# Performance work log

Measured on AMD Instinct MI355X. Metric: run time of the kernel, lower is better.

Reference implementation:

```python
import jax, jax.numpy as jnp
import numpy as np

B, H, W, C = 8, 224, 224, 64
KH = KW = 3          # patch size
RANK = 100           # low rank
FILTERS = 256
IN_DIM = KH * KW * C  # 576


def extract_patches_same(x):
    """tf.image.extract_patches, sizes=3x3, strides=1, rates=1, SAME.

    Output channel ordering matches TF: [kh, kw, C] (spatial-major).
    x: (B,H,W,C) -> (B,H,W,KH*KW*C)
    """
    xp = jnp.pad(x, ((0, 0), (1, 1), (1, 1), (0, 0)))
    slices = [xp[:, di:di + H, dj:dj + W, :]
              for di in range(KH) for dj in range(KW)]
    return jnp.concatenate(slices, axis=-1)


def setup_inputs() -> dict:
    key = jax.random.key(0)
    ks = jax.random.split(key, 11)
    std = 0.05  # keras 'random_normal' initializer stddev
    return {
        "x": jax.random.normal(ks[0], (B, H, W, C), jnp.float32),
        "k": jax.random.normal(ks[1], (IN_DIM, RANK), jnp.float32) * std,
        "l_t": jax.random.normal(ks[2], (RANK, FILTERS), jnp.float32) * std,
        "s": jax.random.normal(ks[3], (RANK, RANK), jnp.float32) * std,
        "aux_U": jax.random.normal(ks[4], (IN_DIM, RANK), jnp.float32) * std,
        "aux_Unp1": jax.random.normal(ks[5], (IN_DIM, RANK), jnp.float32) * std,
        "aux_Vt": jax.random.normal(ks[6], (RANK, FILTERS), jnp.float32) * std,
        "aux_Vtnp1": jax.random.normal(ks[7], (RANK, FILTERS), jnp.float32) * std,
        "b": jax.random.normal(ks[8], (H, W, FILTERS), jnp.float32) * std,
        "aux_b": jax.random.normal(ks[9], (H, W, FILTERS), jnp.float32) * std,
        "step": 2,
    }


def reference(x, k, l_t, s, aux_U, aux_Unp1, aux_Vt, aux_Vtnp1, b, aux_b, step):
    patches = extract_patches_same(x)  # (B,H,W,IN_DIM)
    if step == 0:
        z = jnp.einsum('bhwp,pr->bhwr', patches, k)
        z = jnp.einsum('bhwr,rf->bhwf', z, aux_Vt) + aux_b
    elif step == 1:
        z = jnp.einsum('bhwp,pr->bhwr', patches, aux_U)
        z = jnp.einsum('bhwr,rf->bhwf', z, l_t) + aux_b
    else:
        z = jnp.einsum('bhwp,pr->bhwr', patches, aux_Unp1)
        z = jnp.einsum('bhwr,rq->bhwq', z, s)
        z = jnp.einsum('bhwq,qf->bhwf', z, aux_Vtnp1) + b
    return jax.nn.relu(z)
```

## Files before the change

### kernel.cpp

```cpp
#include <hip/hip_runtime.h>
#include <hip/hip_bf16.h>

#define H_ 224
#define W_ 224
#define C_ 64
#define F_ 256

typedef __attribute__((ext_vector_type(8))) short bf16x8;
typedef __attribute__((ext_vector_type(4))) float f32x4;

__device__ __forceinline__ unsigned short f2bf(float f) {
  union { float f; unsigned int u; } c; c.f = f;
  unsigned int u = c.u;
  return (unsigned short)((u + 0x7fffu + ((u >> 16) & 1u)) >> 16);
}

__global__ __launch_bounds__(256) void prep_kernel(
    const float* __restrict__ Unp1, const float* __restrict__ S,
    const float* __restrict__ Vt,
    unsigned short* __restrict__ uFrag, unsigned short* __restrict__ vFrag) {
  int u = blockIdx.x * 256 + threadIdx.x;
  if (u < 576 * 128) {
    int k = u >> 7;
    int n = u & 127;
    float acc = 0.f;
    if (n < 100) {
      for (int q = 0; q < 100; ++q)
        acc += Unp1[k * 100 + q] * S[q * 100 + n];
    }
    int ks = k >> 5, kk = k & 31, g = kk >> 3, j = kk & 7;
    int nt = n >> 4, lm = n & 15;
    uFrag[(((ks * 8 + nt) * 64) + g * 16 + lm) * 8 + j] = f2bf(acc);
  } else {
    int u2 = u - 576 * 128;
    if (u2 < 4 * 16 * 64 * 8) {
      int j = u2 & 7;
      int lane = (u2 >> 3) & 63;
      int nt = (u2 >> 9) & 15;
      int ks = u2 >> 13;
      int k = ks * 32 + (lane >> 4) * 8 + j;
      int n = nt * 16 + (lane & 15);
      float v = (k < 100) ? Vt[k * 256 + n] : 0.f;
      vFrag[u2] = f2bf(v);
    }
  }
}

__global__ __launch_bounds__(256) void conv_kernel(
    const float* __restrict__ x,
    const unsigned short* __restrict__ uFrag,
    const unsigned short* __restrict__ vFrag,
    const float* __restrict__ bias,
    float* __restrict__ out) {
  __shared__ unsigned short xt[4 * 34 * 64];
  __shared__ unsigned short z1[64 * 128];

  int bid = blockIdx.x;
  int tw = bid % 7;
  int th = (bid / 7) % 112;
  int bb = bid / (7 * 112);
  int h0 = th * 2, w0 = tw * 32;
  int tid = threadIdx.x;
  int lane = tid & 63, wid = tid >> 6;
  int wm = wid & 1, wn = wid >> 1;
  int g = lane >> 4, lm = lane & 15;

  const float* xb = x + (size_t)bb * (H_ * W_ * C_);
  #pragma unroll
  for (int it = 0; it < 5; ++it) {
    int i = tid + it * 256;
    if (i < 1088) {
      int row34 = i >> 3, c8 = i & 7;
      int r = row34 / 34;
      int ww = row34 - r * 34;
      int h = h0 - 1 + r, w = w0 - 1 + ww;
      bf16x8 sv;
      if (h >= 0 && h < H_ && w >= 0 && w < W_) {
        const float* p = xb + ((size_t)(h * W_ + w)) * C_ + c8 * 8;
        float4 f0 = *(const float4*)p;
        float4 f1 = *(const float4*)(p + 4);
        sv[0] = (short)f2bf(f0.x); sv[1] = (short)f2bf(f0.y);
        sv[2] = (short)f2bf(f0.z); sv[3] = (short)f2bf(f0.w);
        sv[4] = (short)f2bf(f1.x); sv[5] = (short)f2bf(f1.y);
        sv[6] = (short)f2bf(f1.z); sv[7] = (short)f2bf(f1.w);
      } else {
        sv = (bf16x8){0, 0, 0, 0, 0, 0, 0, 0};
      }
      *(bf16x8*)&xt[row34 * 64 + ((c8 ^ (row34 & 7)) << 3)] = sv;
    }
  }
  __syncthreads();

  f32x4 acc1[2][4] = {};
  #pragma unroll
  for (int ks = 0; ks < 18; ++ks) {
    int cell = ks >> 1;
    int kh = cell / 3, kw = cell - kh * 3;
    int c0c = (ks & 1) * 4;
    bf16x8 a[2];
    #pragma unroll
    for (int t = 0; t < 2; ++t) {
      int mrow = (2 * wm + t) * 16 + lm;
      int dh = mrow >> 5, dw = mrow & 31;
      int row34 = (dh + kh) * 34 + dw + kw;
      int chunk = (c0c + g) ^ (row34 & 7);
      a[t] = *(const bf16x8*)&xt[row34 * 64 + chunk * 8];
    }
    #pragma unroll
    for (int j = 0; j < 4; ++j) {
      int nt = wn * 4 + j;
      bf16x8 bq = *(const bf16x8*)&uFrag[(((ks * 8 + nt) * 64) + lane) * 8];
      acc1[0][j] = __builtin_amdgcn_mfma_f32_16x16x32_bf16(a[0], bq, acc1[0][j], 0, 0, 0);
      acc1[1][j] = __builtin_amdgcn_mfma_f32_16x16x32_bf16(a[1], bq, acc1[1][j], 0, 0, 0);
    }
  }

  #pragma unroll
  for (int t = 0; t < 2; ++t) {
    #pragma unroll
    for (int j = 0; j < 4; ++j) {
      int col = (wn * 4 + j) * 16 + lm;
      #pragma unroll
      for (int i = 0; i < 4; ++i) {
        int row = (2 * wm + t) * 16 + g * 4 + i;
        z1[row * 128 + (((col >> 3) ^ (row & 7)) << 3) + (col & 7)] = f2bf(acc1[t][j][i]);
      }
    }
  }
  __syncthreads();

  f32x4 acc2[2][8] = {};
  #pragma unroll
  for (int ks = 0; ks < 4; ++ks) {
    bf16x8 a[2];
    #pragma unroll
    for (int t = 0; t < 2; ++t) {
      int row = (2 * wm + t) * 16 + lm;
      int chunk = (ks * 4 + g) ^ (row & 7);
      a[t] = *(const bf16x8*)&z1[row * 128 + chunk * 8];
    }
    #pragma unroll
    for (int j = 0; j < 8; ++j) {
      int nt = wn * 8 + j;
      bf16x8 bq = *(const bf16x8*)&vFrag[(((ks * 16 + nt) * 64) + lane) * 8];
      acc2[0][j] = __builtin_amdgcn_mfma_f32_16x16x32_bf16(a[0], bq, acc2[0][j], 0, 0, 0);
      acc2[1][j] = __builtin_amdgcn_mfma_f32_16x16x32_bf16(a[1], bq, acc2[1][j], 0, 0, 0);
    }
  }

  #pragma unroll
  for (int t = 0; t < 2; ++t) {
    #pragma unroll
    for (int j = 0; j < 8; ++j) {
      int f = (wn * 8 + j) * 16 + lm;
      #pragma unroll
      for (int i = 0; i < 4; ++i) {
        int mrow = (2 * wm + t) * 16 + g * 4 + i;
        int dh = mrow >> 5, dw = mrow & 31;
        int h = h0 + dh, w = w0 + dw;
        size_t po = ((size_t)(h * W_ + w)) * F_ + f;
        float v = acc2[t][j][i] + bias[po];
        out[(size_t)bb * (H_ * W_ * F_) + po] = fmaxf(v, 0.f);
      }
    }
  }
}

extern "C" void kernel_launch(void* const* d_in, const int* in_sizes, int n_in,
                              void* d_out, int out_size, void* d_ws, size_t ws_size,
                              hipStream_t stream) {
  const float* x     = (const float*)d_in[0];
  const float* S     = (const float*)d_in[3];
  const float* Unp1  = (const float*)d_in[5];
  const float* Vtnp1 = (const float*)d_in[7];
  const float* bias  = (const float*)d_in[8];
  float* out = (float*)d_out;

  unsigned short* uFrag = (unsigned short*)d_ws;
  unsigned short* vFrag = (unsigned short*)((char*)d_ws + 18 * 8 * 64 * 8 * 2);

  hipLaunchKernelGGL(prep_kernel, dim3(416), dim3(256), 0, stream,
                     Unp1, S, Vtnp1, uFrag, vFrag);
  hipLaunchKernelGGL(conv_kernel, dim3(8 * 112 * 7), dim3(256), 0, stream,
                     x, uFrag, vFrag, bias, out);
}
```

Measured before the change: 829.4 us.

## Prefetch bias early, split second GEMM, reorder blocks by batch, nontemporal stores

Block indexing is reordered so that consecutive blocks cover the same spatial tile across all 8 batch images, which lets them share bias reads through cache. Bias values are loaded into registers before the MFMA loops so their latency overlaps compute. The second GEMM is split into two halves, each with its own epilogue, to cut accumulator register pressure, and __launch_bounds__(256,4) targets higher occupancy. Output stores use nontemporal hints to avoid polluting cache. The prefetched bias still adds registers, so the occupancy target may force spills.

```diff
diff --git a/kernel.cpp b/kernel.cpp
--- a/kernel.cpp
+++ b/kernel.cpp
@@ -46,7 +46,7 @@
   }
 }
 
-__global__ __launch_bounds__(256) void conv_kernel(
+__global__ __launch_bounds__(256, 4) void conv_kernel(
     const float* __restrict__ x,
     const unsigned short* __restrict__ uFrag,
     const unsigned short* __restrict__ vFrag,
@@ -56,9 +56,10 @@
   __shared__ unsigned short z1[64 * 128];
 
   int bid = blockIdx.x;
-  int tw = bid % 7;
-  int th = (bid / 7) % 112;
-  int bb = bid / (7 * 112);
+  int bb = bid & 7;
+  int t2 = bid >> 3;
+  int tw = t2 % 7;
+  int th = t2 / 7;
   int h0 = th * 2, w0 = tw * 32;
   int tid = threadIdx.x;
   int lane = tid & 63, wid = tid >> 6;
@@ -89,7 +90,28 @@
       *(bf16x8*)&xt[row34 * 64 + ((c8 ^ (row34 & 7)) << 3)] = sv;
     }
   }
+
+  int rowoff[2][4];
+  #pragma unroll
+  for (int t = 0; t < 2; ++t) {
+    #pragma unroll
+    for (int i = 0; i < 4; ++i) {
+      int mrow = (2 * wm + t) * 16 + g * 4 + i;
+      int dh = mrow >> 5, dw = mrow & 31;
+      rowoff[t][i] = (h0 + dh) * W_ + (w0 + dw);
+    }
+  }
+
   __syncthreads();
+
+  float bv0[2][4][4];
+  #pragma unroll
+  for (int t = 0; t < 2; ++t)
+    #pragma unroll
+    for (int j = 0; j < 4; ++j)
+      #pragma unroll
+      for (int i = 0; i < 4; ++i)
+        bv0[t][j][i] = bias[(size_t)rowoff[t][i] * F_ + (wn * 8 + j) * 16 + lm];
 
   f32x4 acc1[2][4] = {};
   #pragma unroll
@@ -129,40 +151,79 @@
   }
   __syncthreads();
 
-  f32x4 acc2[2][8] = {};
-  #pragma unroll
-  for (int ks = 0; ks < 4; ++ks) {
-    bf16x8 a[2];
-    #pragma unroll
-    for (int t = 0; t < 2; ++t) {
-      int row = (2 * wm + t) * 16 + lm;
-      int chunk = (ks * 4 + g) ^ (row & 7);
-      a[t] = *(const bf16x8*)&z1[row * 128 + chunk * 8];
-    }
-    #pragma unroll
-    for (int j = 0; j < 8; ++j) {
-      int nt = wn * 8 + j;
-      bf16x8 bq = *(const bf16x8*)&vFrag[(((ks * 16 + nt) * 64) + lane) * 8];
-      acc2[0][j] = __builtin_amdgcn_mfma_f32_16x16x32_bf16(a[0], bq, acc2[0][j], 0, 0, 0);
-      acc2[1][j] = __builtin_amdgcn_mfma_f32_16x16x32_bf16(a[1], bq, acc2[1][j], 0, 0, 0);
-    }
-  }
-
-  #pragma unroll
-  for (int t = 0; t < 2; ++t) {
-    #pragma unroll
-    for (int j = 0; j < 8; ++j) {
-      int f = (wn * 8 + j) * 16 + lm;
-      #pragma unroll
-      for (int i = 0; i < 4; ++i) {
-        int mrow = (2 * wm + t) * 16 + g * 4 + i;
-        int dh = mrow >> 5, dw = mrow & 31;
-        int h = h0 + dh, w = w0 + dw;
-        size_t po = ((size_t)(h * W_ + w)) * F_ + f;
-        float v = acc2[t][j][i] + bias[po];
-        out[(size_t)bb * (H_ * W_ * F_) + po] = fmaxf(v, 0.f);
-      }
-    }
+  float bv1[2][4][4];
+  #pragma unroll
+  for (int t = 0; t < 2; ++t)
+    #pragma unroll
+    for (int j = 0; j < 4; ++j)
+      #pragma unroll
+      for (int i = 0; i < 4; ++i)
+        bv1[t][j][i] = bias[(size_t)rowoff[t][i] * F_ + (wn * 8 + 4 + j) * 16 + lm];
+
+  float* ob = out + (size_t)bb * (H_ * W_ * F_);
+
+  {
+    f32x4 acc2[2][4] = {};
+    #pragma unroll
+    for (int ks = 0; ks < 4; ++ks) {
+      bf16x8 a[2];
+      #pragma unroll
+      for (int t = 0; t < 2; ++t) {
+        int row = (2 * wm + t) * 16 + lm;
+        int chunk = (ks * 4 + g) ^ (row & 7);
+        a[t] = *(const bf16x8*)&z1[row * 128 + chunk * 8];
+      }
+      #pragma unroll
+      for (int j = 0; j < 4; ++j) {
+        int nt = wn * 8 + j;
+        bf16x8 bq = *(const bf16x8*)&vFrag[(((ks * 16 + nt) * 64) + lane) * 8];
+        acc2[0][j] = __builtin_amdgcn_mfma_f32_16x16x32_bf16(a[0], bq, acc2[0][j], 0, 0, 0);
+        acc2[1][j] = __builtin_amdgcn_mfma_f32_16x16x32_bf16(a[1], bq, acc2[1][j], 0, 0, 0);
+      }
+    }
+    #pragma unroll
+    for (int t = 0; t < 2; ++t)
+      #pragma unroll
+      for (int j = 0; j < 4; ++j) {
+        int f = (wn * 8 + j) * 16 + lm;
+        #pragma unroll
+        for (int i = 0; i < 4; ++i) {
+          float v = fmaxf(acc2[t][j][i] + bv0[t][j][i], 0.f);
+          __builtin_nontemporal_store(v, &ob[(size_t)rowoff[t][i] * F_ + f]);
+        }
+      }
+  }
+
+  {
+    f32x4 acc2[2][4] = {};
+    #pragma unroll
+    for (int ks = 0; ks < 4; ++ks) {
+      bf16x8 a[2];
+      #pragma unroll
+      for (int t = 0; t < 2; ++t) {
+        int row = (2 * wm + t) * 16 + lm;
+        int chunk = (ks * 4 + g) ^ (row & 7);
+        a[t] = *(const bf16x8*)&z1[row * 128 + chunk * 8];
+      }
+      #pragma unroll
+      for (int j = 0; j < 4; ++j) {
+        int nt = wn * 8 + 4 + j;
+        bf16x8 bq = *(const bf16x8*)&vFrag[(((ks * 16 + nt) * 64) + lane) * 8];
+        acc2[0][j] = __builtin_amdgcn_mfma_f32_16x16x32_bf16(a[0], bq, acc2[0][j], 0, 0, 0);
+        acc2[1][j] = __builtin_amdgcn_mfma_f32_16x16x32_bf16(a[1], bq, acc2[1][j], 0, 0, 0);
+      }
+    }
+    #pragma unroll
+    for (int t = 0; t < 2; ++t)
+      #pragma unroll
+      for (int j = 0; j < 4; ++j) {
+        int f = (wn * 8 + 4 + j) * 16 + lm;
+        #pragma unroll
+        for (int i = 0; i < 4; ++i) {
+          float v = fmaxf(acc2[t][j][i] + bv1[t][j][i], 0.f);
+          __builtin_nontemporal_store(v, &ob[(size_t)rowoff[t][i] * F_ + f]);
+        }
+      }
   }
 }
 
```

Result: faster. 792.4 us (-4.5%).

## Loop over batch inside block to reuse bias, remap tiles per XCD

Applied to the files above, without the earlier changes.

Each block now covers one output row of 32 pixels and loops over all 8 batch images. The bias for that tile is loaded into registers once and reused across the batch, instead of being re-read per image. Block indices are remapped so consecutive rows land on the same XCD for L2 locality, and the first GEMM software-prefetches A/B fragments one k-step ahead. The cost is fewer blocks (1568) with more sequential work each, plus a launch-bounds occupancy hint, which risks lower parallelism and latency hiding.

```diff
diff --git a/kernel.cpp b/kernel.cpp
--- a/kernel.cpp
+++ b/kernel.cpp
@@ -46,121 +46,140 @@
   }
 }
 
-__global__ __launch_bounds__(256) void conv_kernel(
+__global__ __launch_bounds__(256, 3) void conv_kernel(
     const float* __restrict__ x,
     const unsigned short* __restrict__ uFrag,
     const unsigned short* __restrict__ vFrag,
     const float* __restrict__ bias,
     float* __restrict__ out) {
-  __shared__ unsigned short xt[4 * 34 * 64];
-  __shared__ unsigned short z1[64 * 128];
+  __shared__ unsigned short xt[3 * 34 * 64];
+  __shared__ unsigned short z1[32 * 128];
 
   int bid = blockIdx.x;
-  int tw = bid % 7;
-  int th = (bid / 7) % 112;
-  int bb = bid / (7 * 112);
-  int h0 = th * 2, w0 = tw * 32;
+  int xcd = bid & 7;
+  int idx = bid >> 3;
+  int tw = idx / 28;
+  int th = xcd * 28 + (idx % 28);
+  int w0 = tw * 32;
+
   int tid = threadIdx.x;
   int lane = tid & 63, wid = tid >> 6;
   int wm = wid & 1, wn = wid >> 1;
   int g = lane >> 4, lm = lane & 15;
-
-  const float* xb = x + (size_t)bb * (H_ * W_ * C_);
+  int wbase = w0 + wm * 16;
+
+  float bv[8][4];
   #pragma unroll
-  for (int it = 0; it < 5; ++it) {
-    int i = tid + it * 256;
-    if (i < 1088) {
-      int row34 = i >> 3, c8 = i & 7;
-      int r = row34 / 34;
-      int ww = row34 - r * 34;
-      int h = h0 - 1 + r, w = w0 - 1 + ww;
-      bf16x8 sv;
-      if (h >= 0 && h < H_ && w >= 0 && w < W_) {
-        const float* p = xb + ((size_t)(h * W_ + w)) * C_ + c8 * 8;
-        float4 f0 = *(const float4*)p;
-        float4 f1 = *(const float4*)(p + 4);
-        sv[0] = (short)f2bf(f0.x); sv[1] = (short)f2bf(f0.y);
-        sv[2] = (short)f2bf(f0.z); sv[3] = (short)f2bf(f0.w);
-        sv[4] = (short)f2bf(f1.x); sv[5] = (short)f2bf(f1.y);
-        sv[6] = (short)f2bf(f1.z); sv[7] = (short)f2bf(f1.w);
-      } else {
-        sv = (bf16x8){0, 0, 0, 0, 0, 0, 0, 0};
-      }
-      *(bf16x8*)&xt[row34 * 64 + ((c8 ^ (row34 & 7)) << 3)] = sv;
-    }
-  }
-  __syncthreads();
-
-  f32x4 acc1[2][4] = {};
-  #pragma unroll
-  for (int ks = 0; ks < 18; ++ks) {
-    int cell = ks >> 1;
-    int kh = cell / 3, kw = cell - kh * 3;
-    int c0c = (ks & 1) * 4;
-    bf16x8 a[2];
-    #pragma unroll
-    for (int t = 0; t < 2; ++t) {
-      int mrow = (2 * wm + t) * 16 + lm;
-      int dh = mrow >> 5, dw = mrow & 31;
-      int row34 = (dh + kh) * 34 + dw + kw;
-      int chunk = (c0c + g) ^ (row34 & 7);
-      a[t] = *(const bf16x8*)&xt[row34 * 64 + chunk * 8];
-    }
-    #pragma unroll
-    for (int j = 0; j < 4; ++j) {
-      int nt = wn * 4 + j;
-      bf16x8 bq = *(const bf16x8*)&uFrag[(((ks * 8 + nt) * 64) + lane) * 8];
-      acc1[0][j] = __builtin_amdgcn_mfma_f32_16x16x32_bf16(a[0], bq, acc1[0][j], 0, 0, 0);
-      acc1[1][j] = __builtin_amdgcn_mfma_f32_16x16x32_bf16(a[1], bq, acc1[1][j], 0, 0, 0);
-    }
-  }
-
-  #pragma unroll
-  for (int t = 0; t < 2; ++t) {
-    #pragma unroll
-    for (int j = 0; j < 4; ++j) {
-      int col = (wn * 4 + j) * 16 + lm;
+  for (int j = 0; j < 8; ++j)
+    #pragma unroll
+    for (int i = 0; i < 4; ++i) {
+      int r = th * W_ + wbase + g * 4 + i;
+      bv[j][i] = bias[(size_t)r * F_ + (wn * 8 + j) * 16 + lm];
+    }
+
+  for (int bb = 0; bb < 8; ++bb) {
+    const float* xb = x + (size_t)bb * (H_ * W_ * C_);
+    #pragma unroll
+    for (int it = 0; it < 4; ++it) {
+      int i = tid + it * 256;
+      if (i < 816) {
+        int row34 = i >> 3, c8 = i & 7;
+        int kh = row34 / 34;
+        int ww = row34 - kh * 34;
+        int h = th - 1 + kh, w = w0 - 1 + ww;
+        bf16x8 sv;
+        if (h >= 0 && h < H_ && w >= 0 && w < W_) {
+          const float* p = xb + ((size_t)(h * W_ + w)) * C_ + c8 * 8;
+          float4 f0 = *(const float4*)p;
+          float4 f1 = *(const float4*)(p + 4);
+          sv[0] = (short)f2bf(f0.x); sv[1] = (short)f2bf(f0.y);
+          sv[2] = (short)f2bf(f0.z); sv[3] = (short)f2bf(f0.w);
+          sv[4] = (short)f2bf(f1.x); sv[5] = (short)f2bf(f1.y);
+          sv[6] = (short)f2bf(f1.z); sv[7] = (short)f2bf(f1.w);
+        } else {
+          sv = (bf16x8){0, 0, 0, 0, 0, 0, 0, 0};
+        }
+        *(bf16x8*)&xt[row34 * 64 + ((c8 ^ (row34 & 7)) << 3)] = sv;
+      }
+    }
+    __syncthreads();
+
+    f32x4 acc1[4] = {};
+    {
+      bf16x8 ae, ao, be[4], bo[4];
+      {
+        int row34 = 0 * 34 + wbase - w0 + lm + 0;
+        int chunk = (0 + g) ^ (row34 & 7);
+        ae = *(const bf16x8*)&xt[row34 * 64 + chunk * 8];
+        #pragma unroll
+        for (int jj = 0; jj < 4; ++jj)
+          be[jj] = *(const bf16x8*)&uFrag[(((0 * 8 + wn * 4 + jj) * 64) + lane) * 8];
+      }
+      #pragma unroll
+      for (int ks = 0; ks < 18; ++ks) {
+        bool even = (ks & 1) == 0;
+        if (ks < 17) {
+          int kn = ks + 1;
+          int cell = kn >> 1;
+          int kh = cell / 3, kw = cell - kh * 3;
+          int row34 = kh * 34 + (wm * 16 + lm) + kw;
+          int chunk = ((kn & 1) * 4 + g) ^ (row34 & 7);
+          bf16x8 a_n = *(const bf16x8*)&xt[row34 * 64 + chunk * 8];
+          if (even) ao = a_n; else ae = a_n;
+          #pragma unroll
+          for (int jj = 0; jj < 4; ++jj) {
+            bf16x8 b_n = *(const bf16x8*)&uFrag[(((kn * 8 + wn * 4 + jj) * 64) + lane) * 8];
+            if (even) bo[jj] = b_n; else be[jj] = b_n;
+          }
+        }
+        #pragma unroll
+        for (int jj = 0; jj < 4; ++jj) {
+          bf16x8 a_c = even ? ae : ao;
+          bf16x8 b_c = even ? be[jj] : bo[jj];
+          acc1[jj] = __builtin_amdgcn_mfma_f32_16x16x32_bf16(a_c, b_c, acc1[jj], 0, 0, 0);
+        }
+      }
+    }
+
+    #pragma unroll
+    for (int jj = 0; jj < 4; ++jj) {
+      int col = (wn * 4 + jj) * 16 + lm;
       #pragma unroll
       for (int i = 0; i < 4; ++i) {
-        int row = (2 * wm + t) * 16 + g * 4 + i;
-        z1[row * 128 + (((col >> 3) ^ (row & 7)) << 3) + (col & 7)] = f2bf(acc1[t][j][i]);
-      }
-    }
-  }
-  __syncthreads();
-
-  f32x4 acc2[2][8] = {};
-  #pragma unroll
-  for (int ks = 0; ks < 4; ++ks) {
-    bf16x8 a[2];
-    #pragma unroll
-    for (int t = 0; t < 2; ++t) {
-      int row = (2 * wm + t) * 16 + lm;
+        int row = wm * 16 + g * 4 + i;
+        z1[row * 128 + (((col >> 3) ^ (row & 7)) << 3) + (col & 7)] = f2bf(acc1[jj][i]);
+      }
+    }
+    __syncthreads();
+
+    f32x4 acc2[8] = {};
+    bf16x8 a2[4];
+    #pragma unroll
+    for (int ks = 0; ks < 4; ++ks) {
+      int row = wm * 16 + lm;
       int chunk = (ks * 4 + g) ^ (row & 7);
-      a[t] = *(const bf16x8*)&z1[row * 128 + chunk * 8];
-    }
-    #pragma unroll
-    for (int j = 0; j < 8; ++j) {
-      int nt = wn * 8 + j;
-      bf16x8 bq = *(const bf16x8*)&vFrag[(((ks * 16 + nt) * 64) + lane) * 8];
-      acc2[0][j] = __builtin_amdgcn_mfma_f32_16x16x32_bf16(a[0], bq, acc2[0][j], 0, 0, 0);
-      acc2[1][j] = __builtin_amdgcn_mfma_f32_16x16x32_bf16(a[1], bq, acc2[1][j], 0, 0, 0);
-    }
-  }
-
-  #pragma unroll
-  for (int t = 0; t < 2; ++t) {
-    #pragma unroll
-    for (int j = 0; j < 8; ++j) {
-      int f = (wn * 8 + j) * 16 + lm;
-      #pragma unroll
-      for (int i = 0; i < 4; ++i) {
-        int mrow = (2 * wm + t) * 16 + g * 4 + i;
-        int dh = mrow >> 5, dw = mrow & 31;
-        int h = h0 + dh, w = w0 + dw;
-        size_t po = ((size_t)(h * W_ + w)) * F_ + f;
-        float v = acc2[t][j][i] + bias[po];
-        out[(size_t)bb * (H_ * W_ * F_) + po] = fmaxf(v, 0.f);
+      a2[ks] = *(const bf16x8*)&z1[row * 128 + chunk * 8];
+    }
+    #pragma unroll
+    for (int ks = 0; ks < 4; ++ks) {
+      bf16x8 bq[8];
+      #pragma unroll
+      for (int j = 0; j < 8; ++j)
+        bq[j] = *(const bf16x8*)&vFrag[(((ks * 16 + wn * 8 + j) * 64) + lane) * 8];
+      #pragma unroll
+      for (int j = 0; j < 8; ++j)
+        acc2[j] = __builtin_amdgcn_mfma_f32_16x16x32_bf16(a2[ks], bq[j], acc2[j], 0, 0, 0);
+    }
+
+    float* ob = out + (size_t)bb * (H_ * W_ * F_) +
+                ((size_t)(th * W_) + wbase) * F_;
+    #pragma unroll
+    for (int i = 0; i < 4; ++i) {
+      int woff = g * 4 + i;
+      #pragma unroll
+      for (int j = 0; j < 8; ++j) {
+        float v = fmaxf(acc2[j][i] + bv[j][i], 0.f);
+        ob[(size_t)woff * F_ + (wn * 8 + j) * 16 + lm] = v;
       }
     }
   }
@@ -181,6 +200,6 @@
 
   hipLaunchKernelGGL(prep_kernel, dim3(416), dim3(256), 0, stream,
                      Unp1, S, Vtnp1, uFrag, vFrag);
-  hipLaunchKernelGGL(conv_kernel, dim3(8 * 112 * 7), dim3(256), 0, stream,
+  hipLaunchKernelGGL(conv_kernel, dim3(224 * 7), dim3(256), 0, stream,
                      x, uFrag, vFrag, bias, out);
 }
```

Result: slower. 1.983 ms (+139.1%).
